# Performance work log

Hardware: AMD Instinct MI355X
Metric: run time of the kernel (lower is better)

Reference implementation:

```python
import jax, jax.numpy as jnp
import numpy as np

N_CAM, C, H, W = 4, 336, 96, 176
D, HB, WB = 6, 240, 120

def setup_inputs() -> dict:
    key = jax.random.key(0)
    k1, k2, k3, k4, k5 = jax.random.split(key, 5)
    return {
        "input": jax.random.normal(k1, (N_CAM, C, H, W), dtype=jnp.float32),
        "projection_u": jax.random.randint(k2, (N_CAM, D, HB, WB), 0, W, dtype=jnp.int32),
        "projection_v": jax.random.randint(k3, (N_CAM, D, HB, WB), 0, H, dtype=jnp.int32),
        "projection_valid": jax.random.randint(k4, (N_CAM, D, HB, WB), 0, 2, dtype=jnp.int32),
        "projection_density": jax.random.uniform(k5, (N_CAM, D, HB, WB), dtype=jnp.float32),
    }

def reference(input, projection_u, projection_v, projection_valid, projection_density):
    """Project2Dto3D: per-voxel gather from each camera feature map at (v,u),
    masked by validity and weighted by density normalization, summed over cameras.
    Output layout: [1, D*C, HB, WB] (336*6 = 2016 channels)."""
    def gather_cam(feat, u, v, valid, dens):
        # feat: (C,H,W); u,v,valid,dens: (D,HB,WB)
        g = feat[:, v, u]                                   # (C,D,HB,WB) gather
        w = valid.astype(feat.dtype) * dens                 # (D,HB,WB)
        return g * w[None]
    per_cam = jax.vmap(gather_cam)(input, projection_u, projection_v,
                                   projection_valid, projection_density)  # (N,C,D,HB,WB)
    out = per_cam.sum(axis=0)                               # (C,D,HB,WB)
    out = jnp.transpose(out, (1, 0, 2, 3))                  # (D,C,HB,WB)
    return out.reshape(1, D * C, HB, WB)
```

## Files before the change

kernel.cpp:

```cpp
#include <hip/hip_runtime.h>

#define NCAM 4
#define C 336
#define H 96
#define W 176
#define D 6
#define HB 240
#define WB 120
#define HW (H * W)
#define CPB 112
#define WBPB 60
#define NCP 3
#define NWP 2

static __device__ __forceinline__ unsigned short f2bf(float f) {
    unsigned u = __float_as_uint(f);
    unsigned r = (u + 0x7fffu + ((u >> 16) & 1u)) >> 16;
    return (unsigned short)r;
}

__global__ __launch_bounds__(256)
void vp_transpose_bf16(const float* __restrict__ in,
                       unsigned short* __restrict__ out) {
    __shared__ float tile[64][33];
    const int cam = blockIdx.z;
    const int hw0 = blockIdx.x * 64;
    const int c0  = blockIdx.y * 32;
    const int tid = threadIdx.x;

    const int hwq = tid & 15;
    const int cl  = tid >> 4;
    const float* src = in + (size_t)cam * C * HW + hw0 + hwq * 4;
#pragma unroll
    for (int cc = 0; cc < 2; ++cc) {
        const int c = c0 + cl + cc * 16;
        if (c < C) {
            const float4 v = *(const float4*)(src + (size_t)c * HW);
            tile[hwq * 4 + 0][cl + cc * 16] = v.x;
            tile[hwq * 4 + 1][cl + cc * 16] = v.y;
            tile[hwq * 4 + 2][cl + cc * 16] = v.z;
            tile[hwq * 4 + 3][cl + cc * 16] = v.w;
        }
    }
    __syncthreads();

    const int hw  = tid >> 2;
    const int oct = tid & 3;
    const int cs  = c0 + oct * 8;
    if (cs < C) {
        uint4 r;
        unsigned* pr = (unsigned*)&r;
#pragma unroll
        for (int k = 0; k < 4; ++k) {
            unsigned lo = f2bf(tile[hw][oct * 8 + 2 * k]);
            unsigned hi = f2bf(tile[hw][oct * 8 + 2 * k + 1]);
            pr[k] = lo | (hi << 16);
        }
        *(uint4*)(out + (size_t)cam * HW * C + (size_t)(hw0 + hw) * C + cs) = r;
    }
}

__global__ __launch_bounds__(256, 4)
void vp_gather_bf16(const unsigned short* __restrict__ tfeat,
                    const int* __restrict__ pu, const int* __restrict__ pv,
                    const int* __restrict__ pvalid,
                    const float* __restrict__ pdens,
                    float* __restrict__ out) {
    __shared__ int   s_off[NCAM][WBPB];
    __shared__ float s_wgt[NCAM][WBPB];

    const int d      = blockIdx.x / HB;
    const int hb     = blockIdx.x % HB;
    const int cpart  = blockIdx.y % NCP;
    const int wbpart = blockIdx.y / NCP;
    const int wb0    = wbpart * WBPB;
    const int tid    = threadIdx.x;

    {
        const int i = tid;
        if (i < NCAM * WBPB) {
            const int cam = i / WBPB, wbl = i % WBPB;
            const size_t pidx =
                ((size_t)(cam * D + d) * HB + hb) * WB + wb0 + wbl;
            s_wgt[cam][wbl] = pvalid[pidx] ? pdens[pidx] : 0.0f;
            s_off[cam][wbl] = cam * (HW * C) + (pv[pidx] * W + pu[pidx]) * C;
        }
    }
    __syncthreads();

    const int wave  = tid >> 6;
    const int lane  = tid & 63;
    const int cq    = lane >> 2;
    const int wbsub = lane & 3;
    const bool cact = (cq < 14);
    const int cqc   = cact ? cq : 13;
    const int cbase = cpart * CPB + cqc * 8;

    uint4 q[4][4];
    int wbc[4];
#pragma unroll
    for (int wbi = 0; wbi < 4; ++wbi) {
        const int wbl = wbsub + 4 * wbi;
        wbc[wbi] = wave * 15 + (wbl < 15 ? wbl : 14);
#pragma unroll
        for (int cam = 0; cam < NCAM; ++cam) {
            q[wbi][cam] =
                *(const uint4*)(tfeat + (size_t)s_off[cam][wbc[wbi]] + cbase);
        }
    }

    float acc[4][8];
#pragma unroll
    for (int i = 0; i < 4; ++i)
#pragma unroll
        for (int j = 0; j < 8; ++j) acc[i][j] = 0.0f;

#pragma unroll
    for (int wbi = 0; wbi < 4; ++wbi) {
#pragma unroll
        for (int cam = 0; cam < NCAM; ++cam) {
            const float w = s_wgt[cam][wbc[wbi]];
            const uint4 v = q[wbi][cam];
            acc[wbi][0] += w * __uint_as_float(v.x << 16);
            acc[wbi][1] += w * __uint_as_float(v.x & 0xffff0000u);
            acc[wbi][2] += w * __uint_as_float(v.y << 16);
            acc[wbi][3] += w * __uint_as_float(v.y & 0xffff0000u);
            acc[wbi][4] += w * __uint_as_float(v.z << 16);
            acc[wbi][5] += w * __uint_as_float(v.z & 0xffff0000u);
            acc[wbi][6] += w * __uint_as_float(v.w << 16);
            acc[wbi][7] += w * __uint_as_float(v.w & 0xffff0000u);
        }
    }

#pragma unroll
    for (int wbi = 0; wbi < 4; ++wbi) {
        const int wbl = wbsub + 4 * wbi;
        if (cact && wbl < 15) {
            const int wb = wb0 + wave * 15 + wbl;
            float* po = out + (((size_t)d * C + cbase) * HB + hb) * WB + wb;
#pragma unroll
            for (int j = 0; j < 8; ++j)
                po[(size_t)j * HB * WB] = acc[wbi][j];
        }
    }
}

extern "C" void kernel_launch(void* const* d_in, const int* in_sizes, int n_in,
                              void* d_out, int out_size, void* d_ws,
                              size_t ws_size, hipStream_t stream) {
    const float* feat  = (const float*)d_in[0];
    const int* pu      = (const int*)d_in[1];
    const int* pv      = (const int*)d_in[2];
    const int* pvalid  = (const int*)d_in[3];
    const float* pdens = (const float*)d_in[4];
    float* out         = (float*)d_out;

    unsigned short* tfeat = (unsigned short*)d_ws;

    dim3 tgrid(HW / 64, (C + 31) / 32, NCAM);
    vp_transpose_bf16<<<tgrid, 256, 0, stream>>>(feat, tfeat);

    dim3 ggrid(D * HB, NCP * NWP);
    vp_gather_bf16<<<ggrid, 256, 0, stream>>>(tfeat, pu, pv, pvalid, pdens,
                                              out);
}
```

Baseline: 199.9 us.

## Loop over channel parts in-block and stage output through LDS for coalesced stores

The gather kernel now processes all three channel parts within one block, so the projection index/weight setup runs once per block instead of three times. It prefetches the next part's bf16 features while accumulating the current one. Results are staged through a shared-memory tile and written as contiguous float2 rows along WB, replacing scattered 4-byte strided stores. This adds shared memory, extra syncthreads, and a third of the previous block count, which could reduce latency hiding.

```diff
diff --git a/kernel.cpp b/kernel.cpp
--- a/kernel.cpp
+++ b/kernel.cpp
@@ -8,9 +8,7 @@
 #define HB 240
 #define WB 120
 #define HW (H * W)
-#define CPB 112
 #define WBPB 60
-#define NCP 3
 #define NWP 2
 
 static __device__ __forceinline__ unsigned short f2bf(float f) {
@@ -68,79 +66,109 @@
                     float* __restrict__ out) {
     __shared__ int   s_off[NCAM][WBPB];
     __shared__ float s_wgt[NCAM][WBPB];
+    __shared__ float s_acc[56][61];
 
-    const int d      = blockIdx.x / HB;
-    const int hb     = blockIdx.x % HB;
-    const int cpart  = blockIdx.y % NCP;
-    const int wbpart = blockIdx.y / NCP;
-    const int wb0    = wbpart * WBPB;
-    const int tid    = threadIdx.x;
+    const int d   = blockIdx.x / HB;
+    const int hb  = blockIdx.x % HB;
+    const int wb0 = blockIdx.y * WBPB;
+    const int tid = threadIdx.x;
 
-    {
-        const int i = tid;
-        if (i < NCAM * WBPB) {
-            const int cam = i / WBPB, wbl = i % WBPB;
-            const size_t pidx =
-                ((size_t)(cam * D + d) * HB + hb) * WB + wb0 + wbl;
-            s_wgt[cam][wbl] = pvalid[pidx] ? pdens[pidx] : 0.0f;
-            s_off[cam][wbl] = cam * (HW * C) + (pv[pidx] * W + pu[pidx]) * C;
-        }
+    if (tid < NCAM * WBPB) {
+        const int cam = tid / WBPB, wbl = tid % WBPB;
+        const size_t pidx = ((size_t)(cam * D + d) * HB + hb) * WB + wb0 + wbl;
+        s_wgt[cam][wbl] = pvalid[pidx] ? pdens[pidx] : 0.0f;
+        s_off[cam][wbl] = cam * (HW * C) + (pv[pidx] * W + pu[pidx]) * C;
     }
     __syncthreads();
 
     const int wave  = tid >> 6;
     const int lane  = tid & 63;
-    const int cq    = lane >> 2;
-    const int wbsub = lane & 3;
+    const int cq    = lane & 15;
+    const int wbsub = lane >> 4;
     const bool cact = (cq < 14);
-    const int cqc   = cact ? cq : 13;
-    const int cbase = cpart * CPB + cqc * 8;
+    const int coff  = (cact ? cq : 13) * 8;
 
-    uint4 q[4][4];
     int wbc[4];
 #pragma unroll
     for (int wbi = 0; wbi < 4; ++wbi) {
         const int wbl = wbsub + 4 * wbi;
         wbc[wbi] = wave * 15 + (wbl < 15 ? wbl : 14);
-#pragma unroll
-        for (int cam = 0; cam < NCAM; ++cam) {
-            q[wbi][cam] =
-                *(const uint4*)(tfeat + (size_t)s_off[cam][wbc[wbi]] + cbase);
-        }
     }
 
-    float acc[4][8];
+    uint4 q[4][4];
 #pragma unroll
-    for (int i = 0; i < 4; ++i)
+    for (int wbi = 0; wbi < 4; ++wbi)
 #pragma unroll
-        for (int j = 0; j < 8; ++j) acc[i][j] = 0.0f;
+        for (int cam = 0; cam < NCAM; ++cam)
+            q[wbi][cam] = *(const uint4*)(tfeat +
+                (size_t)(unsigned)(s_off[cam][wbc[wbi]] + coff));
 
 #pragma unroll
-    for (int wbi = 0; wbi < 4; ++wbi) {
+    for (int cp = 0; cp < 3; ++cp) {
+        float acc[4][8];
 #pragma unroll
-        for (int cam = 0; cam < NCAM; ++cam) {
-            const float w = s_wgt[cam][wbc[wbi]];
-            const uint4 v = q[wbi][cam];
-            acc[wbi][0] += w * __uint_as_float(v.x << 16);
-            acc[wbi][1] += w * __uint_as_float(v.x & 0xffff0000u);
-            acc[wbi][2] += w * __uint_as_float(v.y << 16);
-            acc[wbi][3] += w * __uint_as_float(v.y & 0xffff0000u);
-            acc[wbi][4] += w * __uint_as_float(v.z << 16);
-            acc[wbi][5] += w * __uint_as_float(v.z & 0xffff0000u);
-            acc[wbi][6] += w * __uint_as_float(v.w << 16);
-            acc[wbi][7] += w * __uint_as_float(v.w & 0xffff0000u);
-        }
-    }
+        for (int i = 0; i < 4; ++i)
+#pragma unroll
+            for (int j = 0; j < 8; ++j) acc[i][j] = 0.0f;
 
 #pragma unroll
-    for (int wbi = 0; wbi < 4; ++wbi) {
-        const int wbl = wbsub + 4 * wbi;
-        if (cact && wbl < 15) {
-            const int wb = wb0 + wave * 15 + wbl;
-            float* po = out + (((size_t)d * C + cbase) * HB + hb) * WB + wb;
+        for (int wbi = 0; wbi < 4; ++wbi) {
 #pragma unroll
-            for (int j = 0; j < 8; ++j)
-                po[(size_t)j * HB * WB] = acc[wbi][j];
+            for (int cam = 0; cam < NCAM; ++cam) {
+                const float w = s_wgt[cam][wbc[wbi]];
+                const uint4 v = q[wbi][cam];
+                acc[wbi][0] += w * __uint_as_float(v.x << 16);
+                acc[wbi][1] += w * __uint_as_float(v.x & 0xffff0000u);
+                acc[wbi][2] += w * __uint_as_float(v.y << 16);
+                acc[wbi][3] += w * __uint_as_float(v.y & 0xffff0000u);
+                acc[wbi][4] += w * __uint_as_float(v.z << 16);
+                acc[wbi][5] += w * __uint_as_float(v.z & 0xffff0000u);
+                acc[wbi][6] += w * __uint_as_float(v.w << 16);
+                acc[wbi][7] += w * __uint_as_float(v.w & 0xffff0000u);
+            }
+        }
+
+        if (cp < 2) {
+#pragma unroll
+            for (int wbi = 0; wbi < 4; ++wbi)
+#pragma unroll
+                for (int cam = 0; cam < NCAM; ++cam)
+                    q[wbi][cam] = *(const uint4*)(tfeat +
+                        (size_t)(unsigned)(s_off[cam][wbc[wbi]] + coff +
+                                           (cp + 1) * 112));
+        }
+
+#pragma unroll
+        for (int half = 0; half < 2; ++half) {
+            if (cact && cq >= half * 7 && cq < half * 7 + 7) {
+                const int rbase = (cq - half * 7) * 8;
+#pragma unroll
+                for (int wbi = 0; wbi < 4; ++wbi) {
+                    const int wbl = wbsub + 4 * wbi;
+                    if (wbl < 15) {
+#pragma unroll
+                        for (int j = 0; j < 8; ++j)
+                            s_acc[rbase + j][wave * 15 + wbl] = acc[wbi][j];
+                    }
+                }
+            }
+            __syncthreads();
+
+            const int wp = tid & 31;
+            const int rb = tid >> 5;
+            if (wp < 30) {
+#pragma unroll
+                for (int k = 0; k < 7; ++k) {
+                    const int r = rb + 8 * k;
+                    const int c = cp * 112 + half * 56 + r;
+                    float2 v;
+                    v.x = s_acc[r][wp * 2 + 0];
+                    v.y = s_acc[r][wp * 2 + 1];
+                    *(float2*)(out + (((size_t)d * C + c) * HB + hb) * WB +
+                               wb0 + wp * 2) = v;
+                }
+            }
+            __syncthreads();
         }
     }
 }
@@ -160,7 +188,7 @@
     dim3 tgrid(HW / 64, (C + 31) / 32, NCAM);
     vp_transpose_bf16<<<tgrid, 256, 0, stream>>>(feat, tfeat);
 
-    dim3 ggrid(D * HB, NCP * NWP);
+    dim3 ggrid(D * HB, NWP);
     vp_gather_bf16<<<ggrid, 256, 0, stream>>>(tfeat, pu, pv, pvalid, pdens,
                                               out);
 }
```

After: 182.6 us. -8.7%, faster.
